# Performance work log

Hardware: AMD Instinct MI355X
Metric: run time of the kernel (lower is better)

The kernel has to match this reference:

```python
import jax, jax.numpy as jnp
import numpy as np

LATENT = 256
HEADS = 4
DIM_HEAD = 256            # dim_head = latent_channels
INNER = HEADS * DIM_HEAD  # 1024
ROT_DIM = DIM_HEAD // 2   # rotary dim per coordinate (relative_emb_dim=2)
MIN_FREQ = 1.0 / 64.0     # 1/res
ROT_SCALE = 16.0          # CrossFormer scale
FF_SCALE = 0.5            # Gaussian Fourier feature scale
PI = 3.141592653589793
OUT_CH = 3


def _gelu(x):
    return jax.nn.gelu(x, approximate=False)  # torch nn.GELU default (erf)


def _rot_freqs(coords, dim):
    # coords: [b, n] -> freqs [b, n, dim]
    inv_freq = 1.0 / (10000.0 ** (jnp.arange(0, dim, 2, dtype=jnp.float32) / dim))
    t = coords * (ROT_SCALE / MIN_FREQ)
    f = t[..., None] * inv_freq               # [b, n, dim//2]
    return jnp.concatenate([f, f], axis=-1)    # [b, n, dim]


def _rotate_half(x):
    x1, x2 = jnp.split(x, 2, axis=-1)
    return jnp.concatenate([-x2, x1], axis=-1)


def _apply_rot(t, freqs):
    return t * jnp.cos(freqs) + _rotate_half(t) * jnp.sin(freqs)


def _apply_2d_rot(t, fx, fy):
    d = t.shape[-1]
    tx, ty = t[..., : d // 2], t[..., d // 2 :]
    return jnp.concatenate([_apply_rot(tx, fx), _apply_rot(ty, fy)], axis=-1)


def _inst_norm(t, eps=1e-5):
    # galerkin normalization: non-affine norm over head dim (InstanceNorm1d, affine=False)
    mu = jnp.mean(t, axis=-1, keepdims=True)
    var = jnp.var(t, axis=-1, keepdims=True)
    return (t - mu) * jax.lax.rsqrt(var + eps)


def setup_inputs() -> dict:
    key = jax.random.key(0)
    ks = jax.random.split(key, 20)
    b, nq, nc = 8, 4096, 4096
    s = 0.02
    return {
        "z": jax.random.normal(ks[0], (b, nc, LATENT), jnp.float32),
        "query_pos": jax.random.uniform(ks[1], (b, nq, 2), jnp.float32),
        "context_pos": jax.random.uniform(ks[2], (b, nc, 2), jnp.float32),
        # GaussianFourierFeatureTransform buffer B: [2, mapping_size=latent/2]
        "B_ff": jax.random.normal(ks[3], (2, LATENT // 2), jnp.float32) * FF_SCALE,
        # coordinate_projection linears (bias=False)
        "Wc1": jax.random.normal(ks[4], (LATENT, LATENT), jnp.float32) * s,
        "Wc2": jax.random.normal(ks[5], (LATENT, LATENT), jnp.float32) * s,
        # cross attention projections
        "Wq": jax.random.normal(ks[6], (LATENT, INNER), jnp.float32) * s,
        "Wkv": jax.random.normal(ks[7], (LATENT, 2 * INNER), jnp.float32) * s,
        "Wo": jax.random.normal(ks[8], (INNER, LATENT), jnp.float32) * s,
        "bo": jnp.zeros((LATENT,), jnp.float32),
        # feed-forward (mlp_dim = latent)
        "Wf1": jax.random.normal(ks[9], (LATENT, LATENT), jnp.float32) * s,
        "bf1": jnp.zeros((LATENT,), jnp.float32),
        "Wf2": jax.random.normal(ks[10], (LATENT, LATENT), jnp.float32) * s,
        "bf2": jnp.zeros((LATENT,), jnp.float32),
        # output head
        "Wh1": jax.random.normal(ks[11], (LATENT + 2, LATENT), jnp.float32) * s,
        "Wh2": jax.random.normal(ks[12], (LATENT, LATENT // 2), jnp.float32) * s,
        "Wh3": jax.random.normal(ks[13], (LATENT // 2, OUT_CH), jnp.float32) * s,
        "bh3": jnp.zeros((OUT_CH,), jnp.float32),
    }


def reference(z, query_pos, context_pos, B_ff, Wc1, Wc2, Wq, Wkv, Wo, bo,
              Wf1, bf1, Wf2, bf2, Wh1, Wh2, Wh3, bh3):
    b, nq, _ = query_pos.shape
    nc = z.shape[1]
    # 1) Gaussian Fourier features + 2-layer projection
    ff = 2.0 * PI * (query_pos @ B_ff)                           # [b, nq, latent/2]
    x = jnp.concatenate([jnp.sin(ff), jnp.cos(ff)], axis=-1)      # [b, nq, latent]
    x = _gelu(x @ Wc1) @ Wc2
    # 2) galerkin cross attention with 2D rotary relative pos emb
    q = (x @ Wq).reshape(b, nq, HEADS, DIM_HEAD).transpose(0, 2, 1, 3)
    k, v = jnp.split(z @ Wkv, 2, axis=-1)
    k = k.reshape(b, nc, HEADS, DIM_HEAD).transpose(0, 2, 1, 3)
    v = v.reshape(b, nc, HEADS, DIM_HEAD).transpose(0, 2, 1, 3)
    fxq = _rot_freqs(query_pos[..., 0], ROT_DIM)[:, None]         # [b,1,nq,rot]
    fyq = _rot_freqs(query_pos[..., 1], ROT_DIM)[:, None]
    fxk = _rot_freqs(context_pos[..., 0], ROT_DIM)[:, None]
    fyk = _rot_freqs(context_pos[..., 1], ROT_DIM)[:, None]
    q = _apply_2d_rot(q, fxq, fyq)
    k = _apply_2d_rot(k, fxk, fyk)
    k = _inst_norm(k)
    v = _inst_norm(v)
    kv = jnp.einsum('bhnd,bhne->bhde', k, v)                      # [b,h,d,d]
    attn = jnp.einsum('bhmd,bhde->bhme', q, kv) * (1.0 / nc)      # [b,h,nq,d]
    attn = attn.transpose(0, 2, 1, 3).reshape(b, nq, INNER)
    x = (attn @ Wo + bo) + x                                      # residual
    x = (_gelu(x @ Wf1 + bf1) @ Wf2 + bf2) + x                    # FFN residual
    # 3) output head on [features, coords]
    h = jnp.concatenate([x, query_pos], axis=-1)
    h = _gelu(h @ Wh1)
    h = _gelu(h @ Wh2)
    return h @ Wh3 + bh3                                          # [b, nq, out_ch]
```

## Files before the change

kernel.cpp:

```cpp
#include <hip/hip_runtime.h>
#include <math.h>


typedef unsigned short u16;
typedef __attribute__((ext_vector_type(4))) float f32x4;
typedef __attribute__((ext_vector_type(8))) short s16x8;
typedef __attribute__((ext_vector_type(8))) unsigned short u16x8;
typedef __attribute__((ext_vector_type(4))) unsigned short u16x4;

#define LOG2_1E4_D64 0.20762050593046013f

#define VMCNT(n) do{ asm volatile("s_waitcnt vmcnt(" #n ")" ::: "memory"); \
                     __builtin_amdgcn_sched_barrier(0); }while(0)
#define BARRIER() do{ __builtin_amdgcn_s_barrier(); \
                      __builtin_amdgcn_sched_barrier(0); }while(0)

__device__ __forceinline__ u16 f2b(float f){
  union { float f; unsigned u; } v; v.f = f;
  unsigned u = v.u;
  u += 0x7FFFu + ((u >> 16) & 1u);
  return (u16)(u >> 16);
}
__device__ __forceinline__ float b2f(u16 b){
  union { unsigned u; float f; } v; v.u = ((unsigned)b) << 16; return v.f;
}
__device__ __forceinline__ float gelu_f(float x){
  return 0.5f * x * (1.0f + erff(x * 0.7071067811865475f));
}

#if __has_builtin(__builtin_amdgcn_global_load_lds)
#define HAVE_GLL 1
typedef const __attribute__((address_space(1))) void* as1cv;
typedef __attribute__((address_space(3))) void* as3v;
__device__ __forceinline__ void gload16(const void* g, void* l){
  __builtin_amdgcn_global_load_lds((as1cv)g, (as3v)l, 16, 0, 0);
}
#else
#define HAVE_GLL 0
#endif


struct PrepArgs {
  const float* z; u16* Zb;
  const float* qp; const float* Bff; u16* X0;
  const float* W[9]; u16* Wt[9];
  int K[9]; int N[9]; int boff[10];
  int castB, tcB;
};
__global__ __launch_bounds__(256) void k_prep(PrepArgs a){
  int b = blockIdx.x, tid = threadIdx.x;
  if (b < a.castB){
    long i = (long)b * 256 + tid;
    float4 f = ((const float4*)a.z)[i];
    u16x4 o = { f2b(f.x), f2b(f.y), f2b(f.z), f2b(f.w) };
    ((u16x4*)a.Zb)[i] = o;
  } else if (b < a.castB + a.tcB){
    int bb = b - a.castB;
    int w = 0;
    while (bb >= a.boff[w+1]) w++;
    int idx = (bb - a.boff[w]) * 256 + tid;
    int K = a.K[w], N = a.N[w];
    int n = idx / K, k = idx - n * K;
    a.Wt[w][idx] = f2b(a.W[w][(long)k * N + n]);
  } else {
    int bb = b - a.castB - a.tcB;
    long r = (long)bb * 2 + (tid >> 7);
    int j = tid & 127;
    float qx = a.qp[r*2], qy = a.qp[r*2+1];
    float ff = 6.283185307179586f * (qx * a.Bff[j] + qy * a.Bff[128 + j]);
    a.X0[r*256 + j]       = f2b(sinf(ff));
    a.X0[r*256 + 128 + j] = f2b(cosf(ff));
  }
}

__global__ __launch_bounds__(256) void k_red(const float* __restrict__ p, u16* __restrict__ out,
                                             long stride, float scale){
  long i = (long)blockIdx.x * 256 + threadIdx.x;
  f32x4 s = ((const f32x4*)p)[i];
  s += ((const f32x4*)(p + stride))[i];
  s += ((const f32x4*)(p + 2*stride))[i];
  s += ((const f32x4*)(p + 3*stride))[i];
  u16x4 o = { f2b(s[0]*scale), f2b(s[1]*scale), f2b(s[2]*scale), f2b(s[3]*scale) };
  ((u16x4*)out)[i] = o;
}

__global__ __launch_bounds__(256) void k_final(const u16* __restrict__ H2, const float* __restrict__ Wh3,
                                               const float* __restrict__ bh3, float* __restrict__ out){
  long r = (long)blockIdx.x * 256 + threadIdx.x;
  float a0 = bh3[0], a1 = bh3[1], a2 = bh3[2];
  const u16x8* hrow = (const u16x8*)(H2 + r*128);
#pragma unroll
  for (int c8 = 0; c8 < 16; c8++){
    u16x8 hv = hrow[c8];
#pragma unroll
    for (int e = 0; e < 8; e++){
      float f = b2f(hv[e]);
      int k = c8*8 + e;
      a0 += f * Wh3[k*3];
      a1 += f * Wh3[k*3+1];
      a2 += f * Wh3[k*3+2];
    }
  }
  out[r*3] = a0; out[r*3+1] = a1; out[r*3+2] = a2;
}


template<int MODE>
__global__ __launch_bounds__(256, 2)
void gemm_fuse(const u16* __restrict__ A, const u16* __restrict__ Bw,
               u16* __restrict__ outK, u16* __restrict__ outV,
               const float* __restrict__ pos){
  __shared__ char smem[49152];
  u16* AsB = (u16*)smem;
  u16* BsB = (u16*)(smem + 16384);

  int tid  = threadIdx.x;
  int lane = tid & 63;
  int wave = tid >> 6;
  int wm = (wave & 1) << 6;
  int wn = (wave >> 1) << 7;
  int whalf = wave >> 1;
  int yb = blockIdx.x;
  int h  = yb & 3;
  bool isK = (MODE == 1) || (yb < 4);
  long m0 = (long)blockIdx.y * 128;

  int r15 = lane & 15;
  int cc  = lane >> 4;
  int fsw = (cc ^ ((r15 >> 1) & 3)) * 8;
  const u16* Bh = Bw + (long)yb * 65536;

  f32x4 acc[4][8];
#pragma unroll
  for (int i = 0; i < 4; i++)
#pragma unroll
    for (int j = 0; j < 8; j++)
      acc[i][j] = f32x4{0.f, 0.f, 0.f, 0.f};

#if HAVE_GLL
  int srow  = lane >> 2;
  int scolS = ((lane & 3) ^ ((lane >> 3) & 3)) * 8;
  int aRow[2], bRow[4];
  const u16 *gA[2], *gB[4];
#pragma unroll
  for (int t = 0; t < 2; t++){
    aRow[t] = (wave*2 + t) * 16;
    gA[t] = A + (m0 + aRow[t] + srow) * 256 + scolS;
  }
#pragma unroll
  for (int t = 0; t < 4; t++){
    bRow[t] = (wave*4 + t) * 16;
    gB[t] = Bh + (bRow[t] + srow) * 256 + scolS;
  }
  auto stage = [&](int buf, int kk){
    u16* ab = AsB + buf*4096;
    u16* bb = BsB + buf*8192;
#pragma unroll
    for (int t = 0; t < 2; t++) gload16(gA[t] + kk*32, ab + aRow[t]*32);
#pragma unroll
    for (int t = 0; t < 4; t++) gload16(gB[t] + kk*32, bb + bRow[t]*32);
  };
  auto compute = [&](int buf){
    const u16* ab = AsB + buf*4096;
    const u16* bb = BsB + buf*8192;
    s16x8 af[4], bf[8];
#pragma unroll
    for (int i = 0; i < 4; i++) af[i] = *(const s16x8*)&ab[(wm + i*16 + r15)*32 + fsw];
#pragma unroll
    for (int j = 0; j < 8; j++) bf[j] = *(const s16x8*)&bb[(wn + j*16 + r15)*32 + fsw];
#pragma unroll
    for (int i = 0; i < 4; i++)
#pragma unroll
      for (int j = 0; j < 8; j++)
        acc[i][j] = __builtin_amdgcn_mfma_f32_16x16x32_bf16(af[i], bf[j], acc[i][j], 0, 0, 0);
  };

  stage(0, 0);
  stage(1, 1);
  int cur = 0;
  for (int t = 0; t < 7; t++){
    VMCNT(6);
    BARRIER();
    compute(cur);
    __builtin_amdgcn_sched_barrier(0);
    BARRIER();
    if (t + 2 < 8) stage(cur, t + 2);
    cur ^= 1;
  }
  VMCNT(0);
  BARRIER();
  compute(cur);
#else
  int sm = tid >> 2, sc = tid & 3;
  for (int k0 = 0; k0 < 256; k0 += 32){
    u16x8 va  = *(const u16x8*)(A + (m0 + sm)*256 + sc*8 + k0);
    u16x8 va1 = *(const u16x8*)(A + (m0 + sm + 64)*256 + sc*8 + k0);
    u16x8 vb0 = *(const u16x8*)(Bh + (sm      )*256 + sc*8 + k0);
    u16x8 vb1 = *(const u16x8*)(Bh + (sm + 64 )*256 + sc*8 + k0);
    u16x8 vb2 = *(const u16x8*)(Bh + (sm + 128)*256 + sc*8 + k0);
    u16x8 vb3 = *(const u16x8*)(Bh + (sm + 192)*256 + sc*8 + k0);
    __syncthreads();
    *(u16x8*)&AsB[sm*32 + sc*8] = va;
    *(u16x8*)&AsB[(sm+64)*32 + sc*8] = va1;
    *(u16x8*)&BsB[sm*32 + sc*8] = vb0;
    *(u16x8*)&BsB[(sm+64)*32 + sc*8] = vb1;
    *(u16x8*)&BsB[(sm+128)*32 + sc*8] = vb2;
    *(u16x8*)&BsB[(sm+192)*32 + sc*8] = vb3;
    __syncthreads();
    s16x8 af[4], bf[8];
#pragma unroll
    for (int i = 0; i < 4; i++) af[i] = *(const s16x8*)&AsB[(wm + i*16 + r15)*32 + cc*8];
#pragma unroll
    for (int j = 0; j < 8; j++) bf[j] = *(const s16x8*)&BsB[(wn + j*16 + r15)*32 + cc*8];
#pragma unroll
    for (int i = 0; i < 4; i++)
#pragma unroll
      for (int j = 0; j < 8; j++)
        acc[i][j] = __builtin_amdgcn_mfma_f32_16x16x32_bf16(af[i], bf[j], acc[i][j], 0, 0, 0);
    __syncthreads();
  }
#endif

  if (isK){
    float invf4[4];
#pragma unroll
    for (int jl = 0; jl < 4; jl++)
      invf4[jl] = 1024.0f * exp2f(-(float)(jl*16 + r15) * LOG2_1E4_D64);
#pragma unroll
    for (int i = 0; i < 4; i++){
#pragma unroll
      for (int r = 0; r < 4; r++){
        long n = m0 + wm + i*16 + cc*4 + r;
        float p = pos[n*2 + whalf];
#pragma unroll
        for (int jl = 0; jl < 4; jl++){
          float a = p * invf4[jl];
          float s = __sinf(a), c = __cosf(a);
          float t0 = acc[i][jl][r], t1 = acc[i][jl+4][r];
          acc[i][jl][r]   = t0*c - t1*s;
          acc[i][jl+4][r] = t1*c + t0*s;
        }
      }
    }
  }

  if constexpr (MODE == 1){
    u16* TB = (u16*)smem;
    __syncthreads();
    long rowg = m0;
#pragma unroll
    for (int p = 0; p < 2; p++){
      if ((wave & 1) == p){
#pragma unroll
        for (int i = 0; i < 4; i++)
#pragma unroll
          for (int j = 0; j < 8; j++)
#pragma unroll
            for (int r = 0; r < 4; r++){
              int nl = i*16 + cc*4 + r;
              int d  = wn + j*16 + r15;
              TB[nl*256 + (d ^ ((nl>>2)<<1))] = f2b(acc[i][j][r]);
            }
      }
      __syncthreads();
      {
        int nl = tid >> 2;
        int cb = (tid & 3) * 8;
        int sw = (nl >> 2) << 1;
        int swHi = sw & ~7, swLo = sw & 7;
        u16* orow = outK + (rowg + p*64 + nl) * 1024 + yb*256;
#pragma unroll
        for (int c8 = 0; c8 < 8; c8++){
          int cblk = cb + c8*32;
          u16x8 vv = *(const u16x8*)&TB[nl*256 + (cblk ^ swHi)];
          u16x8 ov;
#pragma unroll
          for (int e = 0; e < 8; e++) ov[e] = vv[e ^ swLo];
          *(u16x8*)(orow + cblk) = ov;
        }
      }
      __syncthreads();
    }
  } else {
    u16*   TB  = (u16*)smem;
    float* PS1 = (float*)(smem + 32768);
    float* PS2 = (float*)(smem + 33792);

    __syncthreads();

#pragma unroll
    for (int i = 0; i < 4; i++){
#pragma unroll
      for (int r = 0; r < 4; r++){
        float s1 = 0.f, s2 = 0.f;
#pragma unroll
        for (int j = 0; j < 8; j++){
          float v = acc[i][j][r];
          s1 += v; s2 += v*v;
        }
#pragma unroll
        for (int m = 1; m < 16; m <<= 1){
          s1 += __shfl_xor(s1, m, 64);
          s2 += __shfl_xor(s2, m, 64);
        }
        int rowid = (wave&1)*64 + i*16 + cc*4 + r;
        if (r15 == 0){ PS1[whalf*128 + rowid] = s1; PS2[whalf*128 + rowid] = s2; }
      }
    }
    __syncthreads();
#pragma unroll
    for (int i = 0; i < 4; i++){
#pragma unroll
      for (int r = 0; r < 4; r++){
        int rowid = (wave&1)*64 + i*16 + cc*4 + r;
        float s1 = PS1[rowid] + PS1[128 + rowid];
        float s2 = PS2[rowid] + PS2[128 + rowid];
        float mu  = s1 * 0.00390625f;
        float var = s2 * 0.00390625f - mu*mu;
        float inv = 1.0f / sqrtf(var + 1e-5f);
#pragma unroll
        for (int j = 0; j < 8; j++)
          acc[i][j][r] = (acc[i][j][r] - mu) * inv;
      }
    }
    __syncthreads();

    u16* outp = isK ? outK : outV;
    int bb  = (int)(m0 >> 12);
    int nn0 = (int)(m0 & 4095);
    long matbase = ((long)(bb*4 + h) * 256) * 4096;
#pragma unroll
    for (int p = 0; p < 2; p++){
      if ((wave & 1) == p){
#pragma unroll
        for (int i = 0; i < 4; i++)
#pragma unroll
          for (int j = 0; j < 8; j++)
#pragma unroll
            for (int r = 0; r < 4; r++){
              int nl = i*16 + cc*4 + r;
              int d  = wn + j*16 + r15;
              TB[nl*256 + (d ^ ((nl>>2)<<1))] = f2b(acc[i][j][r]);
            }
      }
      __syncthreads();
      {
        int n4 = (lane & 15) * 4;
        int sw = (lane & 15) << 1;
#pragma unroll
        for (int rnd = 0; rnd < 16; rnd++){
          int d = rnd*16 + wave*4 + (lane >> 4);
          u16x4 vv;
#pragma unroll
          for (int jj = 0; jj < 4; jj++) vv[jj] = TB[(n4+jj)*256 + (d ^ sw)];
          *(u16x4*)(outp + matbase + (long)d*4096 + nn0 + p*64 + n4) = vv;
        }
      }
      __syncthreads();
    }
  }
}


enum { EP_B = 0, EP_GELU = 1, EP_BIAS_GELU = 2, EP_BIAS_RESB = 3, EP_QP_GELU = 4, EP_F32 = 5 };

struct GArgs {
  const u16* A; const u16* B;
  u16* Cb; float* Cf;
  const float* bias; const u16* res; const float* qp; const float* wtail;
  int M, N, K, lda, ldb, ldc, NLO;
  long sAh, sAl, sBh, sBl, sCh, sCl;
};

template<int EP>
__global__ __launch_bounds__(256, 2)
void gemm_k(GArgs g){
  int z = blockIdx.z;
  int zh = z / g.NLO, zl = z - zh * g.NLO;
  const u16* A = g.A + (long)zh * g.sAh + (long)zl * g.sAl;
  const u16* B = g.B + (long)zh * g.sBh + (long)zl * g.sBl;
  long coff = (long)zh * g.sCh + (long)zl * g.sCl;

  __shared__ u16 As[2][128*32];
  __shared__ u16 Bs[2][128*32];

  int tid  = threadIdx.x;
  int lane = tid & 63;
  int wave = tid >> 6;
  int wm = (wave & 1) << 6;
  int wn = (wave >> 1) << 6;
  long m0 = (long)blockIdx.x * 128;
  long n0 = (long)blockIdx.y * 128;

  int r15 = lane & 15;
  int cc  = lane >> 4;
  int fsw = (cc ^ ((r15 >> 1) & 3)) * 8;

  f32x4 acc[4][4];
#pragma unroll
  for (int i = 0; i < 4; i++)
#pragma unroll
    for (int j = 0; j < 4; j++)
      acc[i][j] = f32x4{0.f, 0.f, 0.f, 0.f};

#if HAVE_GLL
  int srow  = lane >> 2;
  int scolS = ((lane & 3) ^ ((lane >> 3) & 3)) * 8;
  int aRow[2];
  const u16 *gA[2], *gB[2];
#pragma unroll
  for (int t = 0; t < 2; t++){
    aRow[t] = (wave*2 + t) * 16;
    gA[t] = A + (m0 + aRow[t] + srow) * g.lda + scolS;
    gB[t] = B + (n0 + aRow[t] + srow) * g.ldb + scolS;
  }
  auto stage = [&](int buf, int kk){
#pragma unroll
    for (int t = 0; t < 2; t++){
      gload16(gA[t] + kk*32, &As[buf][aRow[t]*32]);
      gload16(gB[t] + kk*32, &Bs[buf][aRow[t]*32]);
    }
  };
  auto compute = [&](int buf){
    s16x8 af[4], bf[4];
#pragma unroll
    for (int i = 0; i < 4; i++) af[i] = *(const s16x8*)&As[buf][(wm + i*16 + r15)*32 + fsw];
#pragma unroll
    for (int i = 0; i < 4; i++) bf[i] = *(const s16x8*)&Bs[buf][(wn + i*16 + r15)*32 + fsw];
#pragma unroll
    for (int i = 0; i < 4; i++)
#pragma unroll
      for (int j = 0; j < 4; j++)
        acc[i][j] = __builtin_amdgcn_mfma_f32_16x16x32_bf16(af[i], bf[j], acc[i][j], 0, 0, 0);
  };

  int nt = g.K >> 5;
  stage(0, 0);
  stage(1, 1);
  int cur = 0;
  for (int t = 0; t < nt - 1; t++){
    VMCNT(4);
    BARRIER();
    compute(cur);
    __builtin_amdgcn_sched_barrier(0);
    BARRIER();
    if (t + 2 < nt) stage(cur, t + 2);
    cur ^= 1;
  }
  VMCNT(0);
  BARRIER();
  compute(cur);
#else
  int sm  = tid >> 2;
  int sc  = tid & 3;
  for (int k0 = 0; k0 < g.K; k0 += 32){
    u16x8 va0 = *(const u16x8*)(A + (m0 + sm )*g.lda + sc*8 + k0);
    u16x8 va1 = *(const u16x8*)(A + (m0 + sm + 64)*g.lda + sc*8 + k0);
    u16x8 vb0 = *(const u16x8*)(B + (n0 + sm )*g.ldb + sc*8 + k0);
    u16x8 vb1 = *(const u16x8*)(B + (n0 + sm + 64)*g.ldb + sc*8 + k0);
    __syncthreads();
    *(u16x8*)&As[0][sm*32 + sc*8] = va0;
    *(u16x8*)&As[0][(sm+64)*32 + sc*8] = va1;
    *(u16x8*)&Bs[0][sm*32 + sc*8] = vb0;
    *(u16x8*)&Bs[0][(sm+64)*32 + sc*8] = vb1;
    __syncthreads();
    s16x8 af[4], bf[4];
#pragma unroll
    for (int i = 0; i < 4; i++) af[i] = *(const s16x8*)&As[0][(wm + i*16 + r15)*32 + cc*8];
#pragma unroll
    for (int i = 0; i < 4; i++) bf[i] = *(const s16x8*)&Bs[0][(wn + i*16 + r15)*32 + cc*8];
#pragma unroll
    for (int i = 0; i < 4; i++)
#pragma unroll
      for (int j = 0; j < 4; j++)
        acc[i][j] = __builtin_amdgcn_mfma_f32_16x16x32_bf16(af[i], bf[j], acc[i][j], 0, 0, 0);
    __syncthreads();
  }
#endif

  int colb = (int)n0 + wn + r15;
  int rowb = (int)m0 + wm + cc * 4;
#pragma unroll
  for (int i = 0; i < 4; i++){
#pragma unroll
    for (int j = 0; j < 4; j++){
      int col = colb + j*16;
#pragma unroll
      for (int r = 0; r < 4; r++){
        int row = rowb + i*16 + r;
        float v = acc[i][j][r];
        if constexpr (EP == EP_B){
          g.Cb[coff + (long)row * g.ldc + col] = f2b(v);
        } else if constexpr (EP == EP_GELU){
          g.Cb[coff + (long)row * g.ldc + col] = f2b(gelu_f(v));
        } else if constexpr (EP == EP_BIAS_GELU){
          v = gelu_f(v + g.bias[col]);
          g.Cb[coff + (long)row * g.ldc + col] = f2b(v);
        } else if constexpr (EP == EP_BIAS_RESB){
          v += g.bias[col] + b2f(g.res[coff + (long)row * g.ldc + col]);
          g.Cb[coff + (long)row * g.ldc + col] = f2b(v);
        } else if constexpr (EP == EP_F32){
          g.Cf[coff + (long)row * g.ldc + col] = v;
        } else {
          v += g.qp[(long)row*2] * g.wtail[col] + g.qp[(long)row*2+1] * g.wtail[256+col];
          g.Cb[coff + (long)row * g.ldc + col] = f2b(gelu_f(v));
        }
      }
    }
  }
}


extern "C" void kernel_launch(void* const* d_in, const int* in_sizes, int n_in,
                              void* d_out, int out_size, void* d_ws, size_t ws_size,
                              hipStream_t stream){
  const float* z   = (const float*)d_in[0];
  const float* qp  = (const float*)d_in[1];
  const float* cp  = (const float*)d_in[2];
  const float* Bff = (const float*)d_in[3];
  const float* Wc1 = (const float*)d_in[4];
  const float* Wc2 = (const float*)d_in[5];
  const float* Wq  = (const float*)d_in[6];
  const float* Wkv = (const float*)d_in[7];
  const float* Wo  = (const float*)d_in[8];
  const float* bo  = (const float*)d_in[9];
  const float* Wf1 = (const float*)d_in[10];
  const float* bf1 = (const float*)d_in[11];
  const float* Wf2 = (const float*)d_in[12];
  const float* bf2 = (const float*)d_in[13];
  const float* Wh1 = (const float*)d_in[14];
  const float* Wh2 = (const float*)d_in[15];
  const float* Wh3 = (const float*)d_in[16];
  const float* bh3 = (const float*)d_in[17];
  float* out = (float*)d_out;
  (void)in_sizes; (void)n_in; (void)out_size;

  size_t mb = ws_size >> 20;
  int C;
  if      (mb >= 268) C = 1;
  else if (mb >= 172) C = 2;
  else if (mb >= 124) C = 4;
  else                C = 8;
  const int NB = 8 / C;
  const long R = (long)NB * 4096;

  char* ws = (char*)d_ws;
  const size_t MB = 1024*1024;
  u16* WqT  = (u16*)(ws + 0);
  u16* WkvT = (u16*)(ws + 512*1024);
  u16* WoT  = (u16*)(ws + 1536*1024);
  u16* Wc1T = (u16*)(ws + 2048*1024);
  u16* Wc2T = (u16*)(ws + (2048+128)*1024);
  u16* Wf1T = (u16*)(ws + (2048+256)*1024);
  u16* Wf2T = (u16*)(ws + (2048+384)*1024);
  u16* Wh1T = (u16*)(ws + (2048+512)*1024);
  u16* Wh2T = (u16*)(ws + (2048+640)*1024);
  u16* R1 = (u16*)(ws + 4*MB);
  u16* R2 = (u16*)(ws + 20*MB);
  u16* R3 = (u16*)(ws + 36*MB);
  u16* R4 = (u16*)(ws + 52*MB);
  u16* kvB = (u16*)(ws + 68*MB);
  u16* W2T = (u16*)(ws + 72*MB);
  u16* BIG1 = (u16*)(ws + 76*MB);
  u16* BIG2 = (u16*)((char*)BIG1 + (size_t)NB*8*MB);
  u16* BIG3 = (u16*)((char*)BIG2 + (size_t)NB*8*MB);

  u16* X0b = R1; u16* X2b = R1;
  u16* Tb  = R2; u16* H1b = R2;
  u16* Xb  = R3;
  u16* Zb  = R4; u16* H2b = R4;

  auto G = [&](int ep, const u16* A, const u16* B, u16* Cb, float* Cf,
               const float* bias, const u16* res, const float* qq, const float* wtail,
               int M, int N, int K, int lda, int ldb, int ldc,
               int nz, int NLO, long sAh, long sAl, long sBh, long sBl, long sCh, long sCl){
    GArgs g;
    g.A=A; g.B=B; g.Cb=Cb; g.Cf=Cf; g.bias=bias; g.res=res; g.qp=qq; g.wtail=wtail;
    g.M=M; g.N=N; g.K=K; g.lda=lda; g.ldb=ldb; g.ldc=ldc; g.NLO=NLO;
    g.sAh=sAh; g.sAl=sAl; g.sBh=sBh; g.sBl=sBl; g.sCh=sCh; g.sCl=sCl;
    dim3 gr(M/128, N/128, nz); dim3 bl(256);
    switch(ep){
      case EP_B:          gemm_k<EP_B><<<gr,bl,0,stream>>>(g); break;
      case EP_GELU:       gemm_k<EP_GELU><<<gr,bl,0,stream>>>(g); break;
      case EP_BIAS_GELU:  gemm_k<EP_BIAS_GELU><<<gr,bl,0,stream>>>(g); break;
      case EP_BIAS_RESB:  gemm_k<EP_BIAS_RESB><<<gr,bl,0,stream>>>(g); break;
      case EP_QP_GELU:    gemm_k<EP_QP_GELU><<<gr,bl,0,stream>>>(g); break;
      case EP_F32:        gemm_k<EP_F32><<<gr,bl,0,stream>>>(g); break;
    }
  };

  {
    PrepArgs a;
    a.z = z; a.Zb = Zb; a.qp = qp; a.Bff = Bff; a.X0 = X0b;
    const float* Ws[9] = { Wq, Wkv, Wo, Wc1, Wc2, Wf1, Wf2, Wh1, Wh2 };
    u16* Wts[9] = { WqT, WkvT, WoT, Wc1T, Wc2T, Wf1T, Wf2T, Wh1T, Wh2T };
    int Ks[9] = { 256, 256, 1024, 256, 256, 256, 256, 256, 256 };
    int Ns[9] = { 1024, 2048, 256, 256, 256, 256, 256, 256, 128 };
    int off = 0;
    for (int i = 0; i < 9; i++){
      a.W[i] = Ws[i]; a.Wt[i] = Wts[i]; a.K[i] = Ks[i]; a.N[i] = Ns[i];
      a.boff[i] = off; off += Ks[i]*Ns[i]/256;
    }
    a.boff[9] = off;
    a.castB = 8192; a.tcB = off;
    k_prep<<<dim3(8192 + off + 16384), dim3(256), 0, stream>>>(a);
  }

  G(EP_GELU, X0b, Wc1T, Tb, 0, 0,0,0,0, 32768,256,256, 256,256,256, 1,1, 0,0,0,0,0,0);
  G(EP_B,    Tb,  Wc2T, Xb, 0, 0,0,0,0, 32768,256,256, 256,256,256, 1,1, 0,0,0,0,0,0);

  for (int c = 0; c < C; c++){
    long row0 = (long)c * R;
    const u16* Zc = Zb + row0 * 256;
    u16* kvC  = kvB + (long)c*NB*262144;
    u16* W2Tc = W2T + (long)c*NB*262144;
    gemm_fuse<0><<<dim3(8, (int)(R/128)), dim3(256), 0, stream>>>(Zc, WkvT, BIG2, BIG3, cp + row0*2);
    G(EP_F32, BIG2, BIG3, 0, (float*)BIG1, 0,0,0,0,
      256,256,1024, 4096,4096,256, 4*NB*4, NB*4,
      1024,1048576, 1024,1048576, (long)NB*4*65536,65536);
    k_red<<<dim3(NB*256), dim3(256), 0, stream>>>((float*)BIG1, kvC, (long)NB*4*65536, 1.0f/4096.0f);
    G(EP_B, WoT, kvC, W2Tc, 0, 0,0,0,0,
      256,256,256, 1024,256,1024, NB*4, 4,
      0,256, 262144,65536, 262144,256);
    gemm_fuse<1><<<dim3(4, (int)(R/128)), dim3(256), 0, stream>>>(Xb + row0*256, WqT, BIG1, 0, qp + row0*2);
    G(EP_BIAS_RESB, BIG1, W2Tc, X2b + row0*256, 0, bo, Xb + row0*256, 0,0,
      4096,256,1024, 1024,1024,256, NB, 1,
      4194304,0, 262144,0, 1048576,0);
  }

  G(EP_BIAS_GELU, X2b, Wf1T, Tb, 0, bf1, 0,0,0, 32768,256,256, 256,256,256, 1,1, 0,0,0,0,0,0);
  G(EP_BIAS_RESB, Tb, Wf2T, Xb, 0, bf2, X2b, 0,0, 32768,256,256, 256,256,256, 1,1, 0,0,0,0,0,0);
  G(EP_QP_GELU, Xb, Wh1T, H1b, 0, 0,0, qp, Wh1 + 65536, 32768,256,256, 256,256,256, 1,1, 0,0,0,0,0,0);
  G(EP_GELU, H1b, Wh2T, H2b, 0, 0,0,0,0, 32768,128,256, 256,256,128, 1,1, 0,0,0,0,0,0);
  k_final<<<dim3(128), dim3(256), 0, stream>>>(H2b, Wh3, bh3, out);
}
```

Before: 550.4 us.

## Fuse back-to-back MLP GEMM pairs into single kernels with LDS-resident intermediate

Adds a two-stage GEMM kernel that computes a 128x256 row tile of the first linear with GELU/bias epilogue, keeps it in swizzled LDS, and immediately multiplies it by the second weight matrix. It replaces the coordinate projection pair, the FFN pair, and the output head (Wh1, Wh2 and the 3-wide Wh3 projection, which is folded in via shuffle reductions). This is meant to remove the global round-trips of the intermediate activations and several launches. In exchange it uses about 67KB of LDS and 32 accumulators per thread, which lowers occupancy, and B operands are read directly from global memory without staging.

```diff
diff --git a/kernel.cpp b/kernel.cpp
--- a/kernel.cpp
+++ b/kernel.cpp
@@ -84,26 +84,6 @@
   ((u16x4*)out)[i] = o;
 }
 
-__global__ __launch_bounds__(256) void k_final(const u16* __restrict__ H2, const float* __restrict__ Wh3,
-                                               const float* __restrict__ bh3, float* __restrict__ out){
-  long r = (long)blockIdx.x * 256 + threadIdx.x;
-  float a0 = bh3[0], a1 = bh3[1], a2 = bh3[2];
-  const u16x8* hrow = (const u16x8*)(H2 + r*128);
-#pragma unroll
-  for (int c8 = 0; c8 < 16; c8++){
-    u16x8 hv = hrow[c8];
-#pragma unroll
-    for (int e = 0; e < 8; e++){
-      float f = b2f(hv[e]);
-      int k = c8*8 + e;
-      a0 += f * Wh3[k*3];
-      a1 += f * Wh3[k*3+1];
-      a2 += f * Wh3[k*3+2];
-    }
-  }
-  out[r*3] = a0; out[r*3+1] = a1; out[r*3+2] = a2;
-}
-
 
 template<int MODE>
 __global__ __launch_bounds__(256, 2)
@@ -362,12 +342,12 @@
 }
 
 
-enum { EP_B = 0, EP_GELU = 1, EP_BIAS_GELU = 2, EP_BIAS_RESB = 3, EP_QP_GELU = 4, EP_F32 = 5 };
+enum { EP_B = 0, EP_BIAS_RESB = 1, EP_F32 = 2 };
 
 struct GArgs {
   const u16* A; const u16* B;
   u16* Cb; float* Cf;
-  const float* bias; const u16* res; const float* qp; const float* wtail;
+  const float* bias; const u16* res;
   int M, N, K, lda, ldb, ldc, NLO;
   long sAh, sAl, sBh, sBl, sCh, sCl;
 };
@@ -491,21 +471,215 @@
         float v = acc[i][j][r];
         if constexpr (EP == EP_B){
           g.Cb[coff + (long)row * g.ldc + col] = f2b(v);
-        } else if constexpr (EP == EP_GELU){
-          g.Cb[coff + (long)row * g.ldc + col] = f2b(gelu_f(v));
-        } else if constexpr (EP == EP_BIAS_GELU){
-          v = gelu_f(v + g.bias[col]);
-          g.Cb[coff + (long)row * g.ldc + col] = f2b(v);
         } else if constexpr (EP == EP_BIAS_RESB){
           v += g.bias[col] + b2f(g.res[coff + (long)row * g.ldc + col]);
           g.Cb[coff + (long)row * g.ldc + col] = f2b(v);
-        } else if constexpr (EP == EP_F32){
+        } else {
           g.Cf[coff + (long)row * g.ldc + col] = v;
+        }
+      }
+    }
+  }
+}
+
+
+struct G2Args {
+  const u16* A; const u16* B1; const u16* B2;
+  const float* bias1; const float* bias2;
+  const u16* res; const float* qpos; const float* wtail;
+  const float* Wh3; const float* bh3;
+  u16* outB; float* outF;
+};
+
+template<int VAR>
+__global__ __launch_bounds__(256, 2)
+void gemm2_k(G2Args g){
+  __shared__ char smem[68608];
+  u16* AsB   = (u16*)smem;
+  u16* Atile = (u16*)smem;
+  float* PS  = (float*)(smem + 65536);
+
+  int tid  = threadIdx.x;
+  int lane = tid & 63;
+  int wave = tid >> 6;
+  int wm = (wave & 1) << 6;
+  int wn = (wave >> 1) << 7;
+  long m0 = (long)blockIdx.x * 128;
+  int r15 = lane & 15;
+  int cc  = lane >> 4;
+  int fsw = (cc ^ ((r15 >> 1) & 3)) * 8;
+
+  f32x4 acc[4][8];
+#pragma unroll
+  for (int i = 0; i < 4; i++)
+#pragma unroll
+    for (int j = 0; j < 8; j++)
+      acc[i][j] = f32x4{0.f, 0.f, 0.f, 0.f};
+
+#if HAVE_GLL
+  {
+    int srow  = lane >> 2;
+    int scolS = ((lane & 3) ^ ((lane >> 3) & 3)) * 8;
+    int aRow[2]; const u16* gA[2];
+#pragma unroll
+    for (int t = 0; t < 2; t++){
+      aRow[t] = (wave*2 + t) * 16;
+      gA[t] = g.A + (m0 + aRow[t] + srow) * 256 + scolS;
+    }
+    auto stageA = [&](int buf, int kk){
+#pragma unroll
+      for (int t = 0; t < 2; t++) gload16(gA[t] + kk*32, AsB + buf*4096 + aRow[t]*32);
+    };
+    stageA(0, 0);
+    __syncthreads();
+    int cur = 0;
+    for (int t = 0; t < 8; t++){
+      if (t < 7) stageA(cur ^ 1, t + 1);
+      int k0 = t * 32;
+      s16x8 af[4], bf[8];
+#pragma unroll
+      for (int i = 0; i < 4; i++) af[i] = *(const s16x8*)&AsB[cur*4096 + (wm + i*16 + r15)*32 + fsw];
+#pragma unroll
+      for (int j = 0; j < 8; j++) bf[j] = *(const s16x8*)(g.B1 + (wn + j*16 + r15)*256 + k0 + cc*8);
+#pragma unroll
+      for (int i = 0; i < 4; i++)
+#pragma unroll
+        for (int j = 0; j < 8; j++)
+          acc[i][j] = __builtin_amdgcn_mfma_f32_16x16x32_bf16(af[i], bf[j], acc[i][j], 0, 0, 0);
+      __syncthreads();
+      cur ^= 1;
+    }
+  }
+#else
+  for (int k0 = 0; k0 < 256; k0 += 32){
+    s16x8 af[4], bf[8];
+#pragma unroll
+    for (int i = 0; i < 4; i++) af[i] = *(const s16x8*)(g.A + (m0 + wm + i*16 + r15)*256 + k0 + cc*8);
+#pragma unroll
+    for (int j = 0; j < 8; j++) bf[j] = *(const s16x8*)(g.B1 + (wn + j*16 + r15)*256 + k0 + cc*8);
+#pragma unroll
+    for (int i = 0; i < 4; i++)
+#pragma unroll
+      for (int j = 0; j < 8; j++)
+        acc[i][j] = __builtin_amdgcn_mfma_f32_16x16x32_bf16(af[i], bf[j], acc[i][j], 0, 0, 0);
+  }
+  __syncthreads();
+#endif
+
+#pragma unroll
+  for (int i = 0; i < 4; i++){
+#pragma unroll
+    for (int j = 0; j < 8; j++){
+#pragma unroll
+      for (int r = 0; r < 4; r++){
+        int row = wm + i*16 + cc*4 + r;
+        int col = wn + j*16 + r15;
+        float v = acc[i][j][r];
+        if constexpr (VAR == 0){
+          v = gelu_f(v);
+        } else if constexpr (VAR == 1){
+          v = gelu_f(v + g.bias1[col]);
         } else {
-          v += g.qp[(long)row*2] * g.wtail[col] + g.qp[(long)row*2+1] * g.wtail[256+col];
-          g.Cb[coff + (long)row * g.ldc + col] = f2b(gelu_f(v));
-        }
-      }
+          long gr = m0 + row;
+          v += g.qpos[gr*2] * g.wtail[col] + g.qpos[gr*2+1] * g.wtail[256+col];
+          v = gelu_f(v);
+        }
+        int colp = ((((col>>3) ^ ((row>>1)&3)) << 3) | (col & 7));
+        Atile[row*256 + colp] = f2b(v);
+      }
+    }
+  }
+  __syncthreads();
+
+  if constexpr (VAR < 2){
+    f32x4 acc2[4][8];
+#pragma unroll
+    for (int i = 0; i < 4; i++)
+#pragma unroll
+      for (int j = 0; j < 8; j++)
+        acc2[i][j] = f32x4{0.f, 0.f, 0.f, 0.f};
+#pragma unroll
+    for (int t = 0; t < 8; t++){
+      int k0 = t * 32;
+      s16x8 af[4], bf[8];
+#pragma unroll
+      for (int i = 0; i < 4; i++) af[i] = *(const s16x8*)&Atile[(wm + i*16 + r15)*256 + k0 + fsw];
+#pragma unroll
+      for (int j = 0; j < 8; j++) bf[j] = *(const s16x8*)(g.B2 + (wn + j*16 + r15)*256 + k0 + cc*8);
+#pragma unroll
+      for (int i = 0; i < 4; i++)
+#pragma unroll
+        for (int j = 0; j < 8; j++)
+          acc2[i][j] = __builtin_amdgcn_mfma_f32_16x16x32_bf16(af[i], bf[j], acc2[i][j], 0, 0, 0);
+    }
+#pragma unroll
+    for (int i = 0; i < 4; i++){
+#pragma unroll
+      for (int j = 0; j < 8; j++){
+#pragma unroll
+        for (int r = 0; r < 4; r++){
+          long row = m0 + wm + i*16 + cc*4 + r;
+          int col = wn + j*16 + r15;
+          float v = acc2[i][j][r];
+          if constexpr (VAR == 1)
+            v += g.bias2[col] + b2f(g.res[row*256 + col]);
+          g.outB[row*256 + col] = f2b(v);
+        }
+      }
+    }
+  } else {
+    int wn2 = (wave >> 1) << 6;
+    f32x4 acc2[4][4];
+#pragma unroll
+    for (int i = 0; i < 4; i++)
+#pragma unroll
+      for (int j = 0; j < 4; j++)
+        acc2[i][j] = f32x4{0.f, 0.f, 0.f, 0.f};
+#pragma unroll
+    for (int t = 0; t < 8; t++){
+      int k0 = t * 32;
+      s16x8 af[4], bf[4];
+#pragma unroll
+      for (int i = 0; i < 4; i++) af[i] = *(const s16x8*)&Atile[(wm + i*16 + r15)*256 + k0 + fsw];
+#pragma unroll
+      for (int j = 0; j < 4; j++) bf[j] = *(const s16x8*)(g.B2 + (wn2 + j*16 + r15)*256 + k0 + cc*8);
+#pragma unroll
+      for (int i = 0; i < 4; i++)
+#pragma unroll
+        for (int j = 0; j < 4; j++)
+          acc2[i][j] = __builtin_amdgcn_mfma_f32_16x16x32_bf16(af[i], bf[j], acc2[i][j], 0, 0, 0);
+    }
+#pragma unroll
+    for (int i = 0; i < 4; i++){
+#pragma unroll
+      for (int r = 0; r < 4; r++){
+        float p0 = 0.f, p1 = 0.f, p2 = 0.f;
+#pragma unroll
+        for (int j = 0; j < 4; j++){
+          int col = wn2 + j*16 + r15;
+          float hv = gelu_f(acc2[i][j][r]);
+          const float* w3 = g.Wh3 + col*3;
+          p0 += hv * w3[0]; p1 += hv * w3[1]; p2 += hv * w3[2];
+        }
+#pragma unroll
+        for (int m = 1; m < 16; m <<= 1){
+          p0 += __shfl_xor(p0, m, 16);
+          p1 += __shfl_xor(p1, m, 16);
+          p2 += __shfl_xor(p2, m, 16);
+        }
+        if (r15 == 0){
+          int rowid = (wave&1)*64 + i*16 + cc*4 + r;
+          float* ps = PS + (wave>>1)*384 + rowid*3;
+          ps[0] = p0; ps[1] = p1; ps[2] = p2;
+        }
+      }
+    }
+    __syncthreads();
+    if (tid < 128){
+      long row = m0 + tid;
+#pragma unroll
+      for (int c = 0; c < 3; c++)
+        g.outF[row*3 + c] = PS[tid*3 + c] + PS[384 + tid*3 + c] + g.bh3[c];
     }
   }
 }
@@ -556,7 +730,6 @@
   u16* Wh1T = (u16*)(ws + (2048+512)*1024);
   u16* Wh2T = (u16*)(ws + (2048+640)*1024);
   u16* R1 = (u16*)(ws + 4*MB);
-  u16* R2 = (u16*)(ws + 20*MB);
   u16* R3 = (u16*)(ws + 36*MB);
   u16* R4 = (u16*)(ws + 52*MB);
   u16* kvB = (u16*)(ws + 68*MB);
@@ -566,25 +739,21 @@
   u16* BIG3 = (u16*)((char*)BIG2 + (size_t)NB*8*MB);
 
   u16* X0b = R1; u16* X2b = R1;
-  u16* Tb  = R2; u16* H1b = R2;
   u16* Xb  = R3;
-  u16* Zb  = R4; u16* H2b = R4;
+  u16* Zb  = R4;
 
   auto G = [&](int ep, const u16* A, const u16* B, u16* Cb, float* Cf,
-               const float* bias, const u16* res, const float* qq, const float* wtail,
+               const float* bias, const u16* res,
                int M, int N, int K, int lda, int ldb, int ldc,
                int nz, int NLO, long sAh, long sAl, long sBh, long sBl, long sCh, long sCl){
     GArgs g;
-    g.A=A; g.B=B; g.Cb=Cb; g.Cf=Cf; g.bias=bias; g.res=res; g.qp=qq; g.wtail=wtail;
+    g.A=A; g.B=B; g.Cb=Cb; g.Cf=Cf; g.bias=bias; g.res=res;
     g.M=M; g.N=N; g.K=K; g.lda=lda; g.ldb=ldb; g.ldc=ldc; g.NLO=NLO;
     g.sAh=sAh; g.sAl=sAl; g.sBh=sBh; g.sBl=sBl; g.sCh=sCh; g.sCl=sCl;
     dim3 gr(M/128, N/128, nz); dim3 bl(256);
     switch(ep){
       case EP_B:          gemm_k<EP_B><<<gr,bl,0,stream>>>(g); break;
-      case EP_GELU:       gemm_k<EP_GELU><<<gr,bl,0,stream>>>(g); break;
-      case EP_BIAS_GELU:  gemm_k<EP_BIAS_GELU><<<gr,bl,0,stream>>>(g); break;
       case EP_BIAS_RESB:  gemm_k<EP_BIAS_RESB><<<gr,bl,0,stream>>>(g); break;
-      case EP_QP_GELU:    gemm_k<EP_QP_GELU><<<gr,bl,0,stream>>>(g); break;
       case EP_F32:        gemm_k<EP_F32><<<gr,bl,0,stream>>>(g); break;
     }
   };
@@ -606,8 +775,21 @@
     k_prep<<<dim3(8192 + off + 16384), dim3(256), 0, stream>>>(a);
   }
 
-  G(EP_GELU, X0b, Wc1T, Tb, 0, 0,0,0,0, 32768,256,256, 256,256,256, 1,1, 0,0,0,0,0,0);
-  G(EP_B,    Tb,  Wc2T, Xb, 0, 0,0,0,0, 32768,256,256, 256,256,256, 1,1, 0,0,0,0,0,0);
+  auto G2 = [&](int var, const u16* A, const u16* B1, const u16* B2,
+                const float* b1, const float* b2, const u16* res,
+                const float* qq, const float* wt, u16* ob, float* of){
+    G2Args a;
+    a.A=A; a.B1=B1; a.B2=B2; a.bias1=b1; a.bias2=b2; a.res=res;
+    a.qpos=qq; a.wtail=wt; a.Wh3=Wh3; a.bh3=bh3; a.outB=ob; a.outF=of;
+    dim3 gr(256); dim3 bl(256);
+    switch(var){
+      case 0: gemm2_k<0><<<gr,bl,0,stream>>>(a); break;
+      case 1: gemm2_k<1><<<gr,bl,0,stream>>>(a); break;
+      case 2: gemm2_k<2><<<gr,bl,0,stream>>>(a); break;
+    }
+  };
+
+  G2(0, X0b, Wc1T, Wc2T, 0,0,0,0,0, Xb, 0);
 
   for (int c = 0; c < C; c++){
     long row0 = (long)c * R;
@@ -615,22 +797,19 @@
     u16* kvC  = kvB + (long)c*NB*262144;
     u16* W2Tc = W2T + (long)c*NB*262144;
     gemm_fuse<0><<<dim3(8, (int)(R/128)), dim3(256), 0, stream>>>(Zc, WkvT, BIG2, BIG3, cp + row0*2);
-    G(EP_F32, BIG2, BIG3, 0, (float*)BIG1, 0,0,0,0,
+    G(EP_F32, BIG2, BIG3, 0, (float*)BIG1, 0,0,
       256,256,1024, 4096,4096,256, 4*NB*4, NB*4,
       1024,1048576, 1024,1048576, (long)NB*4*65536,65536);
     k_red<<<dim3(NB*256), dim3(256), 0, stream>>>((float*)BIG1, kvC, (long)NB*4*65536, 1.0f/4096.0f);
-    G(EP_B, WoT, kvC, W2Tc, 0, 0,0,0,0,
+    G(EP_B, WoT, kvC, W2Tc, 0, 0,0,
       256,256,256, 1024,256,1024, NB*4, 4,
       0,256, 262144,65536, 262144,256);
     gemm_fuse<1><<<dim3(4, (int)(R/128)), dim3(256), 0, stream>>>(Xb + row0*256, WqT, BIG1, 0, qp + row0*2);
-    G(EP_BIAS_RESB, BIG1, W2Tc, X2b + row0*256, 0, bo, Xb + row0*256, 0,0,
+    G(EP_BIAS_RESB, BIG1, W2Tc, X2b + row0*256, 0, bo, Xb + row0*256,
       4096,256,1024, 1024,1024,256, NB, 1,
       4194304,0, 262144,0, 1048576,0);
   }
 
-  G(EP_BIAS_GELU, X2b, Wf1T, Tb, 0, bf1, 0,0,0, 32768,256,256, 256,256,256, 1,1, 0,0,0,0,0,0);
-  G(EP_BIAS_RESB, Tb, Wf2T, Xb, 0, bf2, X2b, 0,0, 32768,256,256, 256,256,256, 1,1, 0,0,0,0,0,0);
-  G(EP_QP_GELU, Xb, Wh1T, H1b, 0, 0,0, qp, Wh1 + 65536, 32768,256,256, 256,256,256, 1,1, 0,0,0,0,0,0);
-  G(EP_GELU, H1b, Wh2T, H2b, 0, 0,0,0,0, 32768,128,256, 256,256,128, 1,1, 0,0,0,0,0,0);
-  k_final<<<dim3(128), dim3(256), 0, stream>>>(H2b, Wh3, bh3, out);
-}
+  G2(1, X2b, Wf1T, Wf2T, bf1, bf2, X2b, 0,0, Xb, 0);
+  G2(2, Xb, Wh1T, Wh2T, 0,0,0, qp, Wh1 + 65536, 0, out);
+}
```

New measurement: 668.5 us. 1.21x slower.

## Restructure GEMM pipeline to single-barrier prefetch and split non-batched GEMM kernel

Applied to the files above, without the earlier changes.

Changes the double-buffered K loop in both GEMM kernels from prefetch-two-ahead with partial vmcnt waits and two barriers to a prefetch-one-ahead scheme: issue the next stage, compute the current buffer, wait for all loads, then one barrier. It also adds a separate non-batched GEMM kernel without z-dimension stride arithmetic for the large per-row GEMMs, moving the GELU and qp epilogues there. The aim is fewer barriers per iteration and less index overhead, at the cost of less load-latency hiding, since each wait drains all outstanding loads.

```diff
diff --git a/kernel.cpp b/kernel.cpp
--- a/kernel.cpp
+++ b/kernel.cpp
@@ -10,7 +10,7 @@
 
 #define LOG2_1E4_D64 0.20762050593046013f
 
-#define VMCNT(n) do{ asm volatile("s_waitcnt vmcnt(" #n ")" ::: "memory"); \
+#define VMCNT0() do{ asm volatile("s_waitcnt vmcnt(0)" ::: "memory"); \
                      __builtin_amdgcn_sched_barrier(0); }while(0)
 #define BARRIER() do{ __builtin_amdgcn_s_barrier(); \
                       __builtin_amdgcn_sched_barrier(0); }while(0)
@@ -176,20 +176,16 @@
   };
 
   stage(0, 0);
-  stage(1, 1);
+  VMCNT0();
+  BARRIER();
   int cur = 0;
-  for (int t = 0; t < 7; t++){
-    VMCNT(6);
+  for (int t = 0; t < 8; t++){
+    if (t + 1 < 8) stage(cur ^ 1, t + 1);
+    compute(cur);
+    VMCNT0();
     BARRIER();
-    compute(cur);
-    __builtin_amdgcn_sched_barrier(0);
-    BARRIER();
-    if (t + 2 < 8) stage(cur, t + 2);
     cur ^= 1;
   }
-  VMCNT(0);
-  BARRIER();
-  compute(cur);
 #else
   int sm = tid >> 2, sc = tid & 3;
   for (int k0 = 0; k0 < 256; k0 += 32){
@@ -362,12 +358,12 @@
 }
 
 
-enum { EP_B = 0, EP_GELU = 1, EP_BIAS_GELU = 2, EP_BIAS_RESB = 3, EP_QP_GELU = 4, EP_F32 = 5 };
+enum { EP_B = 0, EP_BIAS_RESB = 1, EP_F32 = 2 };
 
 struct GArgs {
   const u16* A; const u16* B;
   u16* Cb; float* Cf;
-  const float* bias; const u16* res; const float* qp; const float* wtail;
+  const float* bias; const u16* res;
   int M, N, K, lda, ldb, ldc, NLO;
   long sAh, sAl, sBh, sBl, sCh, sCl;
 };
@@ -436,20 +432,16 @@
 
   int nt = g.K >> 5;
   stage(0, 0);
-  stage(1, 1);
+  VMCNT0();
+  BARRIER();
   int cur = 0;
-  for (int t = 0; t < nt - 1; t++){
-    VMCNT(4);
+  for (int t = 0; t < nt; t++){
+    if (t + 1 < nt) stage(cur ^ 1, t + 1);
+    compute(cur);
+    VMCNT0();
     BARRIER();
-    compute(cur);
-    __builtin_amdgcn_sched_barrier(0);
-    BARRIER();
-    if (t + 2 < nt) stage(cur, t + 2);
     cur ^= 1;
   }
-  VMCNT(0);
-  BARRIER();
-  compute(cur);
 #else
   int sm  = tid >> 2;
   int sc  = tid & 3;
@@ -491,19 +483,146 @@
         float v = acc[i][j][r];
         if constexpr (EP == EP_B){
           g.Cb[coff + (long)row * g.ldc + col] = f2b(v);
-        } else if constexpr (EP == EP_GELU){
-          g.Cb[coff + (long)row * g.ldc + col] = f2b(gelu_f(v));
-        } else if constexpr (EP == EP_BIAS_GELU){
-          v = gelu_f(v + g.bias[col]);
-          g.Cb[coff + (long)row * g.ldc + col] = f2b(v);
         } else if constexpr (EP == EP_BIAS_RESB){
           v += g.bias[col] + b2f(g.res[coff + (long)row * g.ldc + col]);
           g.Cb[coff + (long)row * g.ldc + col] = f2b(v);
-        } else if constexpr (EP == EP_F32){
+        } else {
           g.Cf[coff + (long)row * g.ldc + col] = v;
+        }
+      }
+    }
+  }
+}
+
+
+enum { EPX_GELU = 0, EPX_BIAS_GELU = 1, EPX_BIAS_RESB = 2, EPX_QP_GELU = 3, EPX_B = 4 };
+
+struct GXArgs {
+  const u16* A; const u16* B;
+  u16* Cb;
+  const float* bias; const u16* res; const float* qp; const float* wtail;
+  int M, N, K, lda, ldb, ldc;
+};
+
+template<int EP>
+__global__ __launch_bounds__(256, 2)
+void gemmx_k(GXArgs g){
+  __shared__ u16 As[2][128*32];
+  __shared__ u16 Bs[2][128*32];
+
+  int tid  = threadIdx.x;
+  int lane = tid & 63;
+  int wave = tid >> 6;
+  int wm = (wave & 1) << 6;
+  int wn = (wave >> 1) << 6;
+  long m0 = (long)blockIdx.x * 128;
+  long n0 = (long)blockIdx.y * 128;
+
+  int r15 = lane & 15;
+  int cc  = lane >> 4;
+  int fsw = (cc ^ ((r15 >> 1) & 3)) * 8;
+
+  f32x4 acc[4][4];
+#pragma unroll
+  for (int i = 0; i < 4; i++)
+#pragma unroll
+    for (int j = 0; j < 4; j++)
+      acc[i][j] = f32x4{0.f, 0.f, 0.f, 0.f};
+
+#if HAVE_GLL
+  int srow  = lane >> 2;
+  int scolS = ((lane & 3) ^ ((lane >> 3) & 3)) * 8;
+  int aRow[2];
+  const u16 *gA[2], *gB[2];
+#pragma unroll
+  for (int t = 0; t < 2; t++){
+    aRow[t] = (wave*2 + t) * 16;
+    gA[t] = g.A + (m0 + aRow[t] + srow) * g.lda + scolS;
+    gB[t] = g.B + (n0 + aRow[t] + srow) * g.ldb + scolS;
+  }
+  auto stage = [&](int buf, int kk){
+#pragma unroll
+    for (int t = 0; t < 2; t++){
+      gload16(gA[t] + kk*32, &As[buf][aRow[t]*32]);
+      gload16(gB[t] + kk*32, &Bs[buf][aRow[t]*32]);
+    }
+  };
+  auto compute = [&](int buf){
+    s16x8 af[4], bf[4];
+#pragma unroll
+    for (int i = 0; i < 4; i++) af[i] = *(const s16x8*)&As[buf][(wm + i*16 + r15)*32 + fsw];
+#pragma unroll
+    for (int i = 0; i < 4; i++) bf[i] = *(const s16x8*)&Bs[buf][(wn + i*16 + r15)*32 + fsw];
+#pragma unroll
+    for (int i = 0; i < 4; i++)
+#pragma unroll
+      for (int j = 0; j < 4; j++)
+        acc[i][j] = __builtin_amdgcn_mfma_f32_16x16x32_bf16(af[i], bf[j], acc[i][j], 0, 0, 0);
+  };
+
+  int nt = g.K >> 5;
+  stage(0, 0);
+  VMCNT0();
+  BARRIER();
+  int cur = 0;
+  for (int t = 0; t < nt; t++){
+    if (t + 1 < nt) stage(cur ^ 1, t + 1);
+    compute(cur);
+    VMCNT0();
+    BARRIER();
+    cur ^= 1;
+  }
+#else
+  int sm  = tid >> 2;
+  int sc  = tid & 3;
+  for (int k0 = 0; k0 < g.K; k0 += 32){
+    u16x8 va0 = *(const u16x8*)(g.A + (m0 + sm )*g.lda + sc*8 + k0);
+    u16x8 va1 = *(const u16x8*)(g.A + (m0 + sm + 64)*g.lda + sc*8 + k0);
+    u16x8 vb0 = *(const u16x8*)(g.B + (n0 + sm )*g.ldb + sc*8 + k0);
+    u16x8 vb1 = *(const u16x8*)(g.B + (n0 + sm + 64)*g.ldb + sc*8 + k0);
+    __syncthreads();
+    *(u16x8*)&As[0][sm*32 + sc*8] = va0;
+    *(u16x8*)&As[0][(sm+64)*32 + sc*8] = va1;
+    *(u16x8*)&Bs[0][sm*32 + sc*8] = vb0;
+    *(u16x8*)&Bs[0][(sm+64)*32 + sc*8] = vb1;
+    __syncthreads();
+    s16x8 af[4], bf[4];
+#pragma unroll
+    for (int i = 0; i < 4; i++) af[i] = *(const s16x8*)&As[0][(wm + i*16 + r15)*32 + cc*8];
+#pragma unroll
+    for (int i = 0; i < 4; i++) bf[i] = *(const s16x8*)&Bs[0][(wn + i*16 + r15)*32 + cc*8];
+#pragma unroll
+    for (int i = 0; i < 4; i++)
+#pragma unroll
+      for (int j = 0; j < 4; j++)
+        acc[i][j] = __builtin_amdgcn_mfma_f32_16x16x32_bf16(af[i], bf[j], acc[i][j], 0, 0, 0);
+    __syncthreads();
+  }
+#endif
+
+  int colb = (int)n0 + wn + r15;
+  int rowb = (int)m0 + wm + cc * 4;
+#pragma unroll
+  for (int i = 0; i < 4; i++){
+#pragma unroll
+    for (int j = 0; j < 4; j++){
+      int col = colb + j*16;
+#pragma unroll
+      for (int r = 0; r < 4; r++){
+        int row = rowb + i*16 + r;
+        float v = acc[i][j][r];
+        if constexpr (EP == EPX_B){
+          g.Cb[(long)row * g.ldc + col] = f2b(v);
+        } else if constexpr (EP == EPX_GELU){
+          g.Cb[(long)row * g.ldc + col] = f2b(gelu_f(v));
+        } else if constexpr (EP == EPX_BIAS_GELU){
+          g.Cb[(long)row * g.ldc + col] = f2b(gelu_f(v + g.bias[col]));
+        } else if constexpr (EP == EPX_BIAS_RESB){
+          v += g.bias[col] + b2f(g.res[(long)row * g.ldc + col]);
+          g.Cb[(long)row * g.ldc + col] = f2b(v);
         } else {
           v += g.qp[(long)row*2] * g.wtail[col] + g.qp[(long)row*2+1] * g.wtail[256+col];
-          g.Cb[coff + (long)row * g.ldc + col] = f2b(gelu_f(v));
+          g.Cb[(long)row * g.ldc + col] = f2b(gelu_f(v));
         }
       }
     }
@@ -571,21 +690,33 @@
   u16* Zb  = R4; u16* H2b = R4;
 
   auto G = [&](int ep, const u16* A, const u16* B, u16* Cb, float* Cf,
-               const float* bias, const u16* res, const float* qq, const float* wtail,
+               const float* bias, const u16* res,
                int M, int N, int K, int lda, int ldb, int ldc,
                int nz, int NLO, long sAh, long sAl, long sBh, long sBl, long sCh, long sCl){
     GArgs g;
-    g.A=A; g.B=B; g.Cb=Cb; g.Cf=Cf; g.bias=bias; g.res=res; g.qp=qq; g.wtail=wtail;
+    g.A=A; g.B=B; g.Cb=Cb; g.Cf=Cf; g.bias=bias; g.res=res;
     g.M=M; g.N=N; g.K=K; g.lda=lda; g.ldb=ldb; g.ldc=ldc; g.NLO=NLO;
     g.sAh=sAh; g.sAl=sAl; g.sBh=sBh; g.sBl=sBl; g.sCh=sCh; g.sCl=sCl;
     dim3 gr(M/128, N/128, nz); dim3 bl(256);
     switch(ep){
       case EP_B:          gemm_k<EP_B><<<gr,bl,0,stream>>>(g); break;
-      case EP_GELU:       gemm_k<EP_GELU><<<gr,bl,0,stream>>>(g); break;
-      case EP_BIAS_GELU:  gemm_k<EP_BIAS_GELU><<<gr,bl,0,stream>>>(g); break;
       case EP_BIAS_RESB:  gemm_k<EP_BIAS_RESB><<<gr,bl,0,stream>>>(g); break;
-      case EP_QP_GELU:    gemm_k<EP_QP_GELU><<<gr,bl,0,stream>>>(g); break;
       case EP_F32:        gemm_k<EP_F32><<<gr,bl,0,stream>>>(g); break;
+    }
+  };
+  auto GX = [&](int ep, const u16* A, const u16* B, u16* Cb,
+                const float* bias, const u16* res, const float* qq, const float* wt,
+                int M, int N, int K, int lda, int ldb, int ldc){
+    GXArgs g;
+    g.A=A; g.B=B; g.Cb=Cb; g.bias=bias; g.res=res; g.qp=qq; g.wtail=wt;
+    g.M=M; g.N=N; g.K=K; g.lda=lda; g.ldb=ldb; g.ldc=ldc;
+    dim3 gr(M/128, N/128); dim3 bl(256);
+    switch(ep){
+      case EPX_GELU:      gemmx_k<EPX_GELU><<<gr,bl,0,stream>>>(g); break;
+      case EPX_BIAS_GELU: gemmx_k<EPX_BIAS_GELU><<<gr,bl,0,stream>>>(g); break;
+      case EPX_BIAS_RESB: gemmx_k<EPX_BIAS_RESB><<<gr,bl,0,stream>>>(g); break;
+      case EPX_QP_GELU:   gemmx_k<EPX_QP_GELU><<<gr,bl,0,stream>>>(g); break;
+      case EPX_B:         gemmx_k<EPX_B><<<gr,bl,0,stream>>>(g); break;
     }
   };
 
@@ -606,8 +737,8 @@
     k_prep<<<dim3(8192 + off + 16384), dim3(256), 0, stream>>>(a);
   }
 
-  G(EP_GELU, X0b, Wc1T, Tb, 0, 0,0,0,0, 32768,256,256, 256,256,256, 1,1, 0,0,0,0,0,0);
-  G(EP_B,    Tb,  Wc2T, Xb, 0, 0,0,0,0, 32768,256,256, 256,256,256, 1,1, 0,0,0,0,0,0);
+  GX(EPX_GELU, X0b, Wc1T, Tb, 0,0,0,0, 32768,256,256, 256,256,256);
+  GX(EPX_B,    Tb,  Wc2T, Xb, 0,0,0,0, 32768,256,256, 256,256,256);
 
   for (int c = 0; c < C; c++){
     long row0 = (long)c * R;
@@ -615,22 +746,22 @@
     u16* kvC  = kvB + (long)c*NB*262144;
     u16* W2Tc = W2T + (long)c*NB*262144;
     gemm_fuse<0><<<dim3(8, (int)(R/128)), dim3(256), 0, stream>>>(Zc, WkvT, BIG2, BIG3, cp + row0*2);
-    G(EP_F32, BIG2, BIG3, 0, (float*)BIG1, 0,0,0,0,
+    G(EP_F32, BIG2, BIG3, 0, (float*)BIG1, 0,0,
       256,256,1024, 4096,4096,256, 4*NB*4, NB*4,
       1024,1048576, 1024,1048576, (long)NB*4*65536,65536);
     k_red<<<dim3(NB*256), dim3(256), 0, stream>>>((float*)BIG1, kvC, (long)NB*4*65536, 1.0f/4096.0f);
-    G(EP_B, WoT, kvC, W2Tc, 0, 0,0,0,0,
+    G(EP_B, WoT, kvC, W2Tc, 0, 0,0,
       256,256,256, 1024,256,1024, NB*4, 4,
       0,256, 262144,65536, 262144,256);
     gemm_fuse<1><<<dim3(4, (int)(R/128)), dim3(256), 0, stream>>>(Xb + row0*256, WqT, BIG1, 0, qp + row0*2);
-    G(EP_BIAS_RESB, BIG1, W2Tc, X2b + row0*256, 0, bo, Xb + row0*256, 0,0,
+    G(EP_BIAS_RESB, BIG1, W2Tc, X2b + row0*256, 0, bo, Xb + row0*256,
       4096,256,1024, 1024,1024,256, NB, 1,
       4194304,0, 262144,0, 1048576,0);
   }
 
-  G(EP_BIAS_GELU, X2b, Wf1T, Tb, 0, bf1, 0,0,0, 32768,256,256, 256,256,256, 1,1, 0,0,0,0,0,0);
-  G(EP_BIAS_RESB, Tb, Wf2T, Xb, 0, bf2, X2b, 0,0, 32768,256,256, 256,256,256, 1,1, 0,0,0,0,0,0);
-  G(EP_QP_GELU, Xb, Wh1T, H1b, 0, 0,0, qp, Wh1 + 65536, 32768,256,256, 256,256,256, 1,1, 0,0,0,0,0,0);
-  G(EP_GELU, H1b, Wh2T, H2b, 0, 0,0,0,0, 32768,128,256, 256,256,128, 1,1, 0,0,0,0,0,0);
+  GX(EPX_BIAS_GELU, X2b, Wf1T, Tb, bf1, 0,0,0, 32768,256,256, 256,256,256);
+  GX(EPX_BIAS_RESB, Tb, Wf2T, Xb, bf2, X2b, 0,0, 32768,256,256, 256,256,256);
+  GX(EPX_QP_GELU, Xb, Wh1T, H1b, 0,0, qp, Wh1 + 65536, 32768,256,256, 256,256,256);
+  GX(EPX_GELU, H1b, Wh2T, H2b, 0,0,0,0, 32768,128,256, 256,256,128);
   k_final<<<dim3(128), dim3(256), 0, stream>>>(H2b, Wh3, bh3, out);
 }
```

Result: slower. 562.2 us (+2.1%).
